# Kernel optimization log

Hardware: AMD Instinct MI355X
Metric: run time of the kernel (lower is better)

The kernel has to match this reference:

```python
import jax, jax.numpy as jnp
import numpy as np
import math

B, L, D, H, ITEMS = 256, 200, 64, 2, 10000
HEAD = D // H
LN_EPS = 1e-12


def setup_inputs() -> dict:
    key = jax.random.key(0)
    ks = jax.random.split(key, 12)
    x = jax.random.normal(ks[0], (B, L, D), dtype=jnp.float32)
    attention_mask = jnp.zeros((B, L, L), dtype=jnp.float32)
    # distinct item ids per sequence -> well-conditioned C_sub submatrices
    perm_keys = jax.random.split(ks[1], B)
    seq_item_ids = jax.vmap(lambda k: jax.random.permutation(k, ITEMS)[:L])(perm_keys).astype(jnp.int32)
    # PSD-ish diversity kernel: C = 0.1 * F F^T + I  (guarantees invertible submatrices)
    F = jax.random.normal(ks[2], (ITEMS, 16), dtype=jnp.float32)
    C_kernel = 0.1 * (F @ F.T) + jnp.eye(ITEMS, dtype=jnp.float32)
    s = 1.0 / math.sqrt(D)
    Wq = jax.random.normal(ks[3], (D, D), dtype=jnp.float32) * s
    bq = jnp.zeros((D,), dtype=jnp.float32)
    Wv = jax.random.normal(ks[4], (D, D), dtype=jnp.float32) * s
    bv = jnp.zeros((D,), dtype=jnp.float32)
    Wd = jax.random.normal(ks[5], (D, D), dtype=jnp.float32) * s
    bd = jnp.zeros((D,), dtype=jnp.float32)
    ln_gamma = jnp.ones((D,), dtype=jnp.float32)
    ln_beta = jnp.zeros((D,), dtype=jnp.float32)
    return {"input_tensor": x, "attention_mask": attention_mask,
            "seq_item_ids": seq_item_ids, "C_kernel": C_kernel,
            "Wq": Wq, "bq": bq, "Wv": Wv, "bv": bv, "Wd": Wd, "bd": bd,
            "ln_gamma": ln_gamma, "ln_beta": ln_beta}


def _layer_norm(x, gamma, beta):
    mu = jnp.mean(x, axis=-1, keepdims=True)
    var = jnp.mean(jnp.square(x - mu), axis=-1, keepdims=True)
    return gamma * (x - mu) / jnp.sqrt(var + LN_EPS) + beta


def reference(input_tensor, attention_mask, seq_item_ids, C_kernel,
              Wq, bq, Wv, bv, Wd, bd, ln_gamma, ln_beta):
    x = input_tensor
    S = x @ Wq.T + bq                                    # [B,L,D]
    S2 = S * S
    L_kernel = jnp.einsum('bld,bmd->blm', S2, S2)        # [B,L,L]
    # gather per-sequence diversity submatrix C_sub[b,i,j] = C[ids[b,i], ids[b,j]]
    C_sub = C_kernel[seq_item_ids[:, :, None], seq_item_ids[:, None, :]]
    eye = jnp.eye(L, dtype=x.dtype)
    C_inv = jnp.linalg.inv(C_sub + 1e-4 * eye)
    T = jnp.einsum('blk,bkm->blm', L_kernel, C_inv)      # [B,L,L]
    diag_T = jnp.diagonal(T, axis1=1, axis2=2)           # [B,L]
    # 2x2 determinants of all (i,j) pairs: T_ii*T_jj - T_ij*T_ji
    subdet = diag_T[:, :, None] * diag_T[:, None, :] - T * jnp.swapaxes(T, 1, 2)
    triu = jnp.triu(jnp.ones((L, L), dtype=x.dtype), k=1)
    denom = jnp.sum(subdet * triu, axis=(1, 2), keepdims=True)
    denom = jnp.maximum(denom, 1e-9)
    subprob = subdet / denom
    diag_matrix = diag_T[:, :, None] * eye               # diag_embed
    score = -(subprob + diag_matrix) / math.sqrt(HEAD)
    score = score + attention_mask
    attn = jax.nn.softmax(score, axis=-1)
    V = x @ Wv.T + bv
    ctx = jnp.einsum('blm,bmd->bld', attn, V)
    out = ctx @ Wd.T + bd
    return _layer_norm(out + x, ln_gamma, ln_beta)
```

## Files before the change

### kernel.cpp

```cpp
#include <hip/hip_runtime.h>
#include <hip/hip_bf16.h>
#include <math.h>

#define NB 256
#define LL 200
#define DD 64
#define ITEMS_N 10000
#define RANK 16
#define ALPHA 1.0001f
#define INV_ALPHA (1.0f/1.0001f)
#define INV_SQRT_HEAD 0.17677669529663687f

typedef __attribute__((ext_vector_type(8))) short short8v;
typedef __attribute__((ext_vector_type(4))) float f32x4;

static __device__ __forceinline__ unsigned short f2b(float f) {
    unsigned u = __float_as_uint(f);
    unsigned r = (u + 0x7fffu + ((u >> 16) & 1u)) >> 16;
    return (unsigned short)r;
}
static __device__ __forceinline__ float b2f(unsigned short h) {
    return __uint_as_float(((unsigned)h) << 16);
}

#define OFF_A     0
#define OFF_TB    29952
#define OFF_CL32  (OFF_TB + 0)
#define OFF_U32   (OFF_TB + 4224)
#define OFF_UTL   (OFF_TB + 6400)
#define OFF_XB    (OFF_TB + 20000)
#define OFF_WQB   (OFF_TB + 49952)
#define OFF_WVB   (OFF_TB + 59168)
#define OFF_BQS   (OFF_TB + 68384)
#define OFF_BVS   (OFF_TB + 68640)
#define OFF_UL    126464
#define OFF_UB    139264
#define OFF_PB    145920
#define OFF_MAUG  (OFF_PB + 0)
#define OFF_MINVT (OFF_PB + 2112)
#define OFF_IDSL  (OFF_PB + 3392)
#define OFF_PIV   (OFF_PB + 4192)
#define OFF_INVSQ (OFF_PB + 4256)
#define OFF_IDP   (OFF_PB + 4320)
#define OFF_ZB    152576
#define OFF_UTH   OFF_ZB
#define OFF_DV    159744
#define OFF_RED   160576
#define OFF_SCAL  160704
#define OFF_ZPAD  160720
#define LDS_TOTAL 160784

__global__ __launch_bounds__(1024) void mega_kernel(
        const float* __restrict__ x,    const float* __restrict__ mask,
        const int*   __restrict__ ids,  const float* __restrict__ C,
        const float* __restrict__ Wq,   const float* __restrict__ bq,
        const float* __restrict__ Wv,   const float* __restrict__ bv,
        const float* __restrict__ Wd,   const float* __restrict__ bd,
        const float* __restrict__ gamma,const float* __restrict__ beta,
        unsigned short* __restrict__ Vg, float* __restrict__ out) {
    extern __shared__ char smem[];
    unsigned short* Abuf = (unsigned short*)(smem + OFF_A);
    unsigned short* Tb   = (unsigned short*)(smem + OFF_TB);
    float* Cl32  = (float*)(smem + OFF_CL32);
    float* U32l  = (float*)(smem + OFF_U32);
    unsigned short* xbu  = (unsigned short*)(smem + OFF_XB);
    unsigned short* Wqbu = (unsigned short*)(smem + OFF_WQB);
    unsigned short* Wvbu = (unsigned short*)(smem + OFF_WVB);
    float* bqs   = (float*)(smem + OFF_BQS);
    float* bvs   = (float*)(smem + OFF_BVS);
    float*          Ul   = (float*)(smem + OFF_UL);
    unsigned short* Wdb  = (unsigned short*)(smem + OFF_UL);
    unsigned short* Ub   = (unsigned short*)(smem + OFF_UB);
    unsigned short* Pb   = (unsigned short*)(smem + OFF_PB);
    unsigned short* Zb   = (unsigned short*)(smem + OFF_ZB);
    float* dv   = (float*)(smem + OFF_DV);
    float* red  = (float*)(smem + OFF_RED);
    float* scal = (float*)(smem + OFF_SCAL);
    const short8v* zpad = (const short8v*)(smem + OFF_ZPAD);
    int*   idsl  = (int*)(smem + OFF_IDSL);
    int*   pivots= (int*)(smem + OFF_PIV);
    float* invsqv= (float*)(smem + OFF_INVSQ);
    int*   idpv  = (int*)(smem + OFF_IDP);
    float* Maug  = (float*)(smem + OFF_MAUG);
    float* MinvT = (float*)(smem + OFF_MINVT);

    int t = threadIdx.x;
    int b = blockIdx.x;
    int wv_ = t >> 6, lane = t & 63, fr = lane & 15, g = lane >> 4;

    int ga_ = t >> 5, gc_ = t & 31;
    float cgv;
    {
        int ia = ids[b*LL + ga_];
        int ic = ids[b*LL + gc_];
        cgv = C[(size_t)ia*ITEMS_N + ic];
    }

    {
        float4 z4; z4.x = 0.f; z4.y = 0.f; z4.z = 0.f; z4.w = 0.f;
        float4* tz = (float4*)(smem + OFF_TB + 92800);
        for (int i = t; i < 232; i += 1024) tz[i] = z4;
        float4* zz = (float4*)Zb;
        for (int i = t; i < 448; i += 1024) zz[i] = z4;
        if (t < 4) ((float4*)(smem + OFF_ZPAD))[t] = z4;
        if (t < 64)  ((unsigned*)(smem + OFF_UB + 6400))[t] = 0;
        if (t < 192) {
            int s = t / 12, c2 = t - s*12;
            *(unsigned*)(smem + OFF_UTL + s*448 + 400 + c2*4) = 0;
        }
        for (int i = t; i < 288; i += 1024) ((unsigned*)(smem + OFF_XB + 28800))[i] = 0;
        const float4* x4p = (const float4*)(x + (size_t)b*12800);
        #pragma unroll
        for (int it2 = 0; it2 < 4; ++it2) {
            int i4 = t + it2*1024;
            if (i4 < 3200) {
                float4 v4 = x4p[i4];
                int r = i4 >> 4, k4 = (i4 & 15) << 2;
                unsigned lo = (unsigned)f2b(v4.x) | ((unsigned)f2b(v4.y) << 16);
                unsigned hi = (unsigned)f2b(v4.z) | ((unsigned)f2b(v4.w) << 16);
                *(uint2*)(xbu + r*72 + k4) = make_uint2(lo, hi);
            }
        }
        {
            float4 q4 = ((const float4*)Wq)[t];
            float4 w4 = ((const float4*)Wv)[t];
            int d2 = t >> 4, k4 = (t & 15) << 2;
            unsigned qlo = (unsigned)f2b(q4.x) | ((unsigned)f2b(q4.y) << 16);
            unsigned qhi = (unsigned)f2b(q4.z) | ((unsigned)f2b(q4.w) << 16);
            *(uint2*)(Wqbu + d2*72 + k4) = make_uint2(qlo, qhi);
            unsigned vlo = (unsigned)f2b(w4.x) | ((unsigned)f2b(w4.y) << 16);
            unsigned vhi = (unsigned)f2b(w4.z) | ((unsigned)f2b(w4.w) << 16);
            *(uint2*)(Wvbu + d2*72 + k4) = make_uint2(vlo, vhi);
        }
        if (t < 64) { bqs[t] = bq[t]; bvs[t] = bv[t]; }
        if (t < LL) idsl[t] = ids[b*LL + t];
        Cl32[ga_*33 + gc_] = cgv;
    }
    __syncthreads();

    unsigned vpack[8];
    #pragma unroll
    for (int it2 = 0; it2 < 4; ++it2) {
        int tile = wv_ + 16*it2;
        vpack[2*it2] = 0; vpack[2*it2 + 1] = 0;
        if (tile < 52) {
            int R = tile >> 2, Dt = tile & 3;
            const char* ar = (const char*)smem + OFF_XB + (R*16 + fr)*144;
            const char* qr = (const char*)smem + OFF_WQB + (Dt*16 + fr)*144;
            const char* vr = (const char*)smem + OFF_WVB + (Dt*16 + fr)*144;
            short8v a0 = *(const short8v*)(ar + g*16);
            short8v a1 = *(const short8v*)(ar + 64 + g*16);
            f32x4 qa = {0.f,0.f,0.f,0.f};
            f32x4 va = {0.f,0.f,0.f,0.f};
            qa = __builtin_amdgcn_mfma_f32_16x16x32_bf16(a0, *(const short8v*)(qr + g*16), qa, 0,0,0);
            qa = __builtin_amdgcn_mfma_f32_16x16x32_bf16(a1, *(const short8v*)(qr + 64 + g*16), qa, 0,0,0);
            va = __builtin_amdgcn_mfma_f32_16x16x32_bf16(a0, *(const short8v*)(vr + g*16), va, 0,0,0);
            va = __builtin_amdgcn_mfma_f32_16x16x32_bf16(a1, *(const short8v*)(vr + 64 + g*16), va, 0,0,0);
            int col = Dt*16 + fr;
            float bqc = bqs[col], bvc = bvs[col];
            #pragma unroll
            for (int reg = 0; reg < 4; ++reg) {
                int row = R*16 + g*4 + reg;
                float sv = qa[reg] + bqc;
                Abuf[row*72 + col] = (row < LL) ? f2b(sv*sv) : (unsigned short)0;
            }
            vpack[2*it2]     = (unsigned)f2b(va[0] + bvc) | ((unsigned)f2b(va[1] + bvc) << 16);
            vpack[2*it2 + 1] = (unsigned)f2b(va[2] + bvc) | ((unsigned)f2b(va[3] + bvc) << 16);
        }
    }
    __syncthreads();

    if (wv_ == 0) {
        int a = lane & 31;
        float diag = Cl32[a*33 + a] - 1.0f;
        float ur[16];
        int   mypiv = 0; float myinv = 0.f;
        bool  removed = false;
        #pragma unroll
        for (int s = 0; s < RANK; ++s) {
            float v = removed ? -3e38f : diag;
            int idx = a;
            #pragma unroll
            for (int off = 16; off > 0; off >>= 1) {
                float v2 = __shfl_xor(v, off);
                int   i2 = __shfl_xor(idx, off);
                if (v2 > v || (v2 == v && i2 < idx)) { v = v2; idx = i2; }
            }
            int p = idx; float dp = v;
            float iv = (dp < 1e-9f) ? 0.0f : (1.0f/sqrtf(dp));
            float c = Cl32[a*33 + p] - ((a == p) ? 1.0f : 0.0f);
            #pragma unroll
            for (int k = 0; k < s; ++k) {
                float upk = __shfl(ur[k], p);
                c -= ur[k] * upk;
            }
            float u = c * iv;
            ur[s] = u;
            diag -= u*u;
            if (a == p) removed = true;
            if (lane == s) { mypiv = p; myinv = iv; }
        }
        #pragma unroll
        for (int s = 0; s < RANK; ++s) U32l[a*17 + s] = ur[s];
        if (lane < 16) {
            pivots[lane] = mypiv;
            invsqv[lane] = myinv;
            idpv[lane]   = idsl[mypiv];
        }
    } else {
        for (int idx = wv_ - 1; idx < 45; idx += 15) {
            int R = 2 + idx/13, Cc = idx % 13;
            short8v a0 = *(const short8v*)((char*)Abuf + (R*16 + fr)*144 + g*16);
            short8v a1 = *(const short8v*)((char*)Abuf + (R*16 + fr)*144 + 64 + g*16);
            short8v b0 = *(const short8v*)((char*)Abuf + (Cc*16 + fr)*144 + g*16);
            short8v b1 = *(const short8v*)((char*)Abuf + (Cc*16 + fr)*144 + 64 + g*16);
            f32x4 acc = {0.f, 0.f, 0.f, 0.f};
            acc = __builtin_amdgcn_mfma_f32_16x16x32_bf16(a0, b0, acc, 0, 0, 0);
            acc = __builtin_amdgcn_mfma_f32_16x16x32_bf16(a1, b1, acc, 0, 0, 0);
            int col = Cc*16 + fr;
            #pragma unroll
            for (int reg = 0; reg < 4; ++reg) {
                int row = R*16 + g*4 + reg;
                if (row < LL && col < LL) Tb[row*232 + col] = f2b(acc[reg]);
            }
        }
    }
    __syncthreads();

    if (wv_ < 4) {
        if (t < LL) {
            int myrow = idsl[t];
            float cg[16];
            #pragma unroll
            for (int s = 0; s < RANK; ++s)
                cg[s] = C[(size_t)myrow*ITEMS_N + idpv[s]];
            float ur[16];
            #pragma unroll
            for (int s = 0; s < RANK; ++s) {
                int p = pivots[s];
                float c = cg[s] - ((t == p) ? 1.0f : 0.0f);
                #pragma unroll
                for (int k = 0; k < s; ++k) c -= ur[k] * U32l[p*17 + k];
                ur[s] = c * invsqv[s];
            }
            unsigned short* Uth = (unsigned short*)(smem + OFF_UTH);
            unsigned short* Utl = (unsigned short*)(smem + OFF_UTL);
            #pragma unroll
            for (int s = 0; s < RANK; ++s) {
                float v = ur[s];
                Ul[t*RANK + s] = v;
                unsigned short hv = f2b(v);
                Ub[t*RANK + s] = hv;
                Uth[s*224 + t] = hv;
                Utl[s*224 + t] = f2b(v - b2f(hv));
            }
        }
    } else {
        for (int idx = 45 + (wv_ - 4); idx < 110; idx += 12) {
            int R = 2 + idx/13, Cc = idx % 13;
            short8v a0 = *(const short8v*)((char*)Abuf + (R*16 + fr)*144 + g*16);
            short8v a1 = *(const short8v*)((char*)Abuf + (R*16 + fr)*144 + 64 + g*16);
            short8v b0 = *(const short8v*)((char*)Abuf + (Cc*16 + fr)*144 + g*16);
            short8v b1 = *(const short8v*)((char*)Abuf + (Cc*16 + fr)*144 + 64 + g*16);
            f32x4 acc = {0.f, 0.f, 0.f, 0.f};
            acc = __builtin_amdgcn_mfma_f32_16x16x32_bf16(a0, b0, acc, 0, 0, 0);
            acc = __builtin_amdgcn_mfma_f32_16x16x32_bf16(a1, b1, acc, 0, 0, 0);
            int col = Cc*16 + fr;
            #pragma unroll
            for (int reg = 0; reg < 4; ++reg) {
                int row = R*16 + g*4 + reg;
                if (row < LL && col < LL) Tb[row*232 + col] = f2b(acc[reg]);
            }
        }
    }
    __syncthreads();

    if (wv_ == 0) {
        const char* uh  = smem + OFF_UTH;
        const char* ul2 = smem + OFF_UTL;
        f32x4 macc = {0.f,0.f,0.f,0.f};
        #pragma unroll
        for (int kb = 0; kb < 7; ++kb) {
            short8v h  = *(const short8v*)(uh  + fr*448 + kb*64 + g*16);
            short8v l2 = *(const short8v*)(ul2 + fr*448 + kb*64 + g*16);
            macc = __builtin_amdgcn_mfma_f32_16x16x32_bf16(h,  h,  macc, 0,0,0);
            macc = __builtin_amdgcn_mfma_f32_16x16x32_bf16(h,  l2, macc, 0,0,0);
            macc = __builtin_amdgcn_mfma_f32_16x16x32_bf16(l2, h,  macc, 0,0,0);
        }
        #pragma unroll
        for (int reg = 0; reg < 4; ++reg) {
            int r = g*4 + reg;
            Maug[r*33 + fr] = macc[reg] + ((r == fr) ? ALPHA : 0.f);
        }
        float m_[16], inv_[16];
        int rl = lane & 15;
        #pragma unroll
        for (int c = 0; c < 16; ++c) {
            m_[c]   = Maug[rl*33 + c];
            inv_[c] = (rl == c) ? 1.0f : 0.0f;
        }
        #pragma unroll
        for (int s = 0; s < 16; ++s) {
            float pv = __shfl(m_[s], s);
            float pvinv = 1.0f / pv;
            float f = m_[s];
            #pragma unroll
            for (int c = 0; c < 16; ++c) {
                float prow = __shfl(m_[c], s) * pvinv;
                float pinv = __shfl(inv_[c], s) * pvinv;
                if (lane == s) { m_[c] = prow; inv_[c] = pinv; }
                else { m_[c] = fmaf(-f, prow, m_[c]); inv_[c] = fmaf(-f, pinv, inv_[c]); }
            }
        }
        if (lane < 16) {
            #pragma unroll
            for (int c = 0; c < 16; ++c) MinvT[c*20 + rl] = inv_[c];
        }
    } else {
        for (int i = t - 64; i < 2720; i += 960) {
            int r = 30 + (i >> 4), c2 = i & 15;
            *(unsigned*)(smem + OFF_TB + r*464 + 400 + c2*4) = 0;
        }
        for (int idx = 110 + (wv_ - 1); idx < 143; idx += 15) {
            int R = 2 + idx/13, Cc = idx % 13;
            short8v a0 = *(const short8v*)((char*)Abuf + (R*16 + fr)*144 + g*16);
            short8v a1 = *(const short8v*)((char*)Abuf + (R*16 + fr)*144 + 64 + g*16);
            short8v b0 = *(const short8v*)((char*)Abuf + (Cc*16 + fr)*144 + g*16);
            short8v b1 = *(const short8v*)((char*)Abuf + (Cc*16 + fr)*144 + 64 + g*16);
            f32x4 acc = {0.f, 0.f, 0.f, 0.f};
            acc = __builtin_amdgcn_mfma_f32_16x16x32_bf16(a0, b0, acc, 0, 0, 0);
            acc = __builtin_amdgcn_mfma_f32_16x16x32_bf16(a1, b1, acc, 0, 0, 0);
            int col = Cc*16 + fr;
            #pragma unroll
            for (int reg = 0; reg < 4; ++reg) {
                int row = R*16 + g*4 + reg;
                if (row < LL && col < LL) Tb[row*232 + col] = f2b(acc[reg]);
            }
        }
    }
    __syncthreads();

    for (int idx = t; idx < LL*RANK; idx += 1024) {
        int i = idx >> 4, r = idx & 15;
        float acc = 0.f;
        #pragma unroll
        for (int k = 0; k < 16; ++k) acc = fmaf(Ul[i*RANK + k], MinvT[r*20 + k], acc);
        Zb[r*224 + i] = f2b(acc);
    }
    if (t < 480) {
        int r = t >> 4, c2 = t & 15;
        *(unsigned*)(smem + OFF_TB + r*464 + 400 + c2*4) = 0;
    }
    for (int u2 = wv_; u2 < 26; u2 += 16) {
        int R = u2 / 13, Cc = u2 - R*13;
        short8v a0 = *(const short8v*)((char*)Abuf + (R*16 + fr)*144 + g*16);
        short8v a1 = *(const short8v*)((char*)Abuf + (R*16 + fr)*144 + 64 + g*16);
        short8v b0 = *(const short8v*)((char*)Abuf + (Cc*16 + fr)*144 + g*16);
        short8v b1 = *(const short8v*)((char*)Abuf + (Cc*16 + fr)*144 + 64 + g*16);
        f32x4 acc = {0.f, 0.f, 0.f, 0.f};
        acc = __builtin_amdgcn_mfma_f32_16x16x32_bf16(a0, b0, acc, 0, 0, 0);
        acc = __builtin_amdgcn_mfma_f32_16x16x32_bf16(a1, b1, acc, 0, 0, 0);
        int col = Cc*16 + fr;
        #pragma unroll
        for (int reg = 0; reg < 4; ++reg) {
            int row = R*16 + g*4 + reg;
            if (row < LL && col < LL) Tb[row*232 + col] = f2b(acc[reg]);
        }
    }
    __syncthreads();

    {
        unsigned short* Vt = Abuf;
        #pragma unroll
        for (int it2 = 0; it2 < 4; ++it2) {
            int tile = wv_ + 16*it2;
            if (tile < 52) {
                int R = tile >> 2, Dt = tile & 3;
                int row0 = R*16 + g*4;
                if (row0 < LL) {
                    *(uint2*)&Vt[(Dt*16 + fr)*232 + row0] =
                        make_uint2(vpack[2*it2], vpack[2*it2 + 1]);
                }
            }
        }
        for (int i = t; i < 2048; i += 1024) {
            int d = i >> 5, mc = i & 31;
            Vt[d*232 + 200 + mc] = 0;
        }
        for (int i = t; i < 4096; i += 1024) {
            int dd = i >> 6, k = i & 63;
            Wdb[dd*72 + k] = f2b(Wd[i]);
        }
    }
    for (int strip = wv_; strip < 13; strip += 16) {
        f32x4 acc = {0.f, 0.f, 0.f, 0.f};
        const char* arow = (const char*)Tb + (size_t)(strip*16 + fr)*464;
        const char* brow = (const char*)Zb + (size_t)fr*448;
        #pragma unroll
        for (int kt = 0; kt < 7; ++kt) {
            short8v a  = *(const short8v*)(arow + kt*64 + g*16);
            short8v bb = *(const short8v*)(brow + kt*64 + g*16);
            acc = __builtin_amdgcn_mfma_f32_16x16x32_bf16(a, bb, acc, 0, 0, 0);
        }
        #pragma unroll
        for (int reg = 0; reg < 4; ++reg) {
            int prow = strip*16 + g*4 + reg;
            Pb[prow*16 + fr] = f2b(acc[reg]);
        }
    }
    __syncthreads();

    float2 mkr0[7];
    {
        int sp = wv_;
        int l0 = sp*16 + g;
        const float* mbase = mask + (size_t)b*40000;
        #pragma unroll
        for (int e = 0; e < 7; ++e) {
            int m0 = 2*fr + 32*e;
            mkr0[e] = ((sp < 13) && (m0 < LL))
                ? *(const float2*)(mbase + (size_t)l0*200 + m0) : make_float2(0.f, 0.f);
        }
    }
    {
        float ps = 0.f, psd = 0.f;
        for (int u = wv_; u < 91; u += 16) {
            int R, Cc;
            if (u < 13) { R = u; Cc = u; }
            else {
                int q = u - 13, rr = 0;
                while (q >= 12 - rr) { q -= 12 - rr; ++rr; }
                R = rr; Cc = rr + 1 + q;
            }
            const short8v* pPR = (g < 2) ? (const short8v*)((const char*)Pb + (R*16 + fr)*32 + g*16) : zpad;
            const short8v* pUC = (g < 2) ? (const short8v*)((const char*)Ub + (Cc*16 + fr)*32 + g*16) : zpad;
            const short8v* pUR = (g < 2) ? (const short8v*)((const char*)Ub + (R*16 + fr)*32 + g*16) : zpad;
            const short8v* pPC = (g < 2) ? (const short8v*)((const char*)Pb + (Cc*16 + fr)*32 + g*16) : zpad;
            f32x4 acc1 = {0.f,0.f,0.f,0.f};
            f32x4 acc2 = {0.f,0.f,0.f,0.f};
            acc1 = __builtin_amdgcn_mfma_f32_16x16x32_bf16(*pPR, *pUC, acc1, 0,0,0);
            acc2 = __builtin_amdgcn_mfma_f32_16x16x32_bf16(*pUR, *pPC, acc2, 0,0,0);
            if (u < 13) {
                #pragma unroll
                for (int reg = 0; reg < 4; ++reg) {
                    int row = R*16 + g*4 + reg, col = Cc*16 + fr;
                    float lk = b2f(Tb[row*232 + col]);
                    float tvA = (lk - acc1[reg]) * INV_ALPHA;
                    float tvT = (lk - acc2[reg]) * INV_ALPHA;
                    if (row < LL && col < LL) {
                        float w = tvA * tvT;
                        Tb[row*232 + col] = f2b(w);
                        ps += w;
                        if (row == col) { dv[row] = tvA; psd += tvA; }
                    }
                }
            } else {
                int col = Cc*16 + fr;
                unsigned short hv[4];
                #pragma unroll
                for (int reg = 0; reg < 4; ++reg) {
                    int row = R*16 + g*4 + reg;
                    float lk = b2f(Tb[row*232 + col]);
                    float tvA = (lk - acc1[reg]) * INV_ALPHA;
                    float tvT = (lk - acc2[reg]) * INV_ALPHA;
                    float w = tvA * tvT;
                    hv[reg] = f2b(w);
                    if (col < LL) {
                        Tb[row*232 + col] = hv[reg];
                        ps += 2.0f * w;
                    }
                }
                if (col < LL) {
                    int row0 = R*16 + g*4;
                    uint2 pk;
                    pk.x = (unsigned)hv[0] | ((unsigned)hv[1] << 16);
                    pk.y = (unsigned)hv[2] | ((unsigned)hv[3] << 16);
                    *(uint2*)&Tb[col*232 + row0] = pk;
                }
            }
        }
        #pragma unroll
        for (int off = 32; off > 0; off >>= 1) {
            ps  += __shfl_xor(ps, off);
            psd += __shfl_xor(psd, off);
        }
        if (lane == 0) { red[wv_] = ps; red[16 + wv_] = psd; }
        __syncthreads();
        if (t == 0) {
            float s1 = 0.f, s2 = 0.f;
            for (int k = 0; k < 16; ++k) { s1 += red[k]; s2 += red[16 + k]; }
            float dn = fmaxf(0.5f*(s2*s2 - s1), 1e-9f);
            scal[0] = 1.0f / dn;
        }
        __syncthreads();
    }

    {
        const unsigned short* Vt = Abuf;
        float invden = scal[0];
        int sp = wv_;
        if (sp < 13) {
            float2 mkr1[7], mkr2[7], mkr3[7];
            {
                const float* mbase = mask + (size_t)b*40000;
                int l1 = sp*16 + 4 + g;
                int l2 = sp*16 + 8 + g, l3 = sp*16 + 12 + g;
                #pragma unroll
                for (int e = 0; e < 7; ++e) {
                    int m0 = 2*fr + 32*e;
                    bool mm = (m0 < LL);
                    mkr1[e] = mm              ? *(const float2*)(mbase + (size_t)l1*200 + m0) : make_float2(0.f, 0.f);
                    mkr2[e] = (mm && l2 < LL) ? *(const float2*)(mbase + (size_t)l2*200 + m0) : make_float2(0.f, 0.f);
                    mkr3[e] = (mm && l3 < LL) ? *(const float2*)(mbase + (size_t)l3*200 + m0) : make_float2(0.f, 0.f);
                }
            }
            float bdv[4], gv[4], bev[4];
            #pragma unroll
            for (int d2 = 0; d2 < 4; ++d2) {
                bdv[d2] = bd[d2*16 + fr];
                gv[d2]  = gamma[d2*16 + fr];
                bev[d2] = beta[d2*16 + fr];
            }
            char* hb = smem + OFF_UB + wv_*1152;
            float2 dvv[7];
            #pragma unroll
            for (int e = 0; e < 7; ++e) {
                int m0 = 2*fr + 32*e;
                dvv[e] = (m0 < LL) ? *(const float2*)(dv + m0) : make_float2(0.f, 0.f);
            }
            auto dorow = [&](const float2 (&mk)[7], int l) {
                if (l < LL) {
                    float dl = dv[l];
                    float sc[14]; float mx = -3e38f;
                    #pragma unroll
                    for (int e = 0; e < 7; ++e) {
                        int m0 = 2*fr + 32*e;
                        if (m0 < LL) {
                            unsigned w2 = *(const unsigned*)((const char*)Tb + ((size_t)l*232 + m0)*2);
                            float w0 = b2f((unsigned short)(w2 & 0xffffu));
                            float w1 = b2f((unsigned short)(w2 >> 16));
                            float s0 = -(fmaf(dl, dvv[e].x, -w0)*invden
                                         + ((m0 == l) ? dl : 0.f))*INV_SQRT_HEAD + mk[e].x;
                            float s1 = -(fmaf(dl, dvv[e].y, -w1)*invden
                                         + ((m0 + 1 == l) ? dl : 0.f))*INV_SQRT_HEAD + mk[e].y;
                            sc[2*e] = s0; sc[2*e + 1] = s1;
                            mx = fmaxf(mx, fmaxf(s0, s1));
                        } else { sc[2*e] = -3e38f; sc[2*e + 1] = -3e38f; }
                    }
                    mx = fmaxf(mx, __shfl_xor(mx, 1));
                    mx = fmaxf(mx, __shfl_xor(mx, 2));
                    mx = fmaxf(mx, __shfl_xor(mx, 4));
                    mx = fmaxf(mx, __shfl_xor(mx, 8));
                    float sum = 0.f;
                    #pragma unroll
                    for (int e = 0; e < 7; ++e) {
                        int m0 = 2*fr + 32*e;
                        if (m0 < LL) {
                            float e0 = __expf(sc[2*e] - mx);
                            float e1 = __expf(sc[2*e + 1] - mx);
                            sc[2*e] = e0; sc[2*e + 1] = e1;
                            sum += e0 + e1;
                        }
                    }
                    sum += __shfl_xor(sum, 1);
                    sum += __shfl_xor(sum, 2);
                    sum += __shfl_xor(sum, 4);
                    sum += __shfl_xor(sum, 8);
                    float isum = 1.0f / sum;
                    #pragma unroll
                    for (int e = 0; e < 7; ++e) {
                        int m0 = 2*fr + 32*e;
                        if (m0 < LL) {
                            unsigned pw = (unsigned)f2b(sc[2*e]*isum)
                                        | ((unsigned)f2b(sc[2*e + 1]*isum) << 16);
                            *(unsigned*)((char*)Tb + ((size_t)l*232 + m0)*2) = pw;
                        }
                    }
                }
            };
            dorow(mkr0, sp*16 + g);
            dorow(mkr1, sp*16 + 4 + g);
            dorow(mkr2, sp*16 + 8 + g);
            dorow(mkr3, sp*16 + 12 + g);
            float xp[16];
            #pragma unroll
            for (int d2 = 0; d2 < 4; ++d2)
                #pragma unroll
                for (int reg = 0; reg < 4; ++reg) {
                    int l = sp*16 + g*4 + reg;
                    xp[d2*4 + reg] = (l < LL)
                        ? x[((size_t)b*LL + l)*64 + d2*16 + fr] : 0.f;
                }
            f32x4 cacc[4];
            #pragma unroll
            for (int d2 = 0; d2 < 4; ++d2) { f32x4 z = {0.f,0.f,0.f,0.f}; cacc[d2] = z; }
            {
                const char* arow = (const char*)Tb + (size_t)(sp*16 + fr)*464;
                #pragma unroll
                for (int kt = 0; kt < 7; ++kt) {
                    short8v a = *(const short8v*)(arow + kt*64 + g*16);
                    #pragma unroll
                    for (int d2 = 0; d2 < 4; ++d2) {
                        short8v bb = *(const short8v*)((const char*)Vt + (d2*16 + fr)*464 + kt*64 + g*16);
                        cacc[d2] = __builtin_amdgcn_mfma_f32_16x16x32_bf16(a, bb, cacc[d2], 0, 0, 0);
                    }
                }
            }
            f32x4 oacc[4];
            #pragma unroll
            for (int d2 = 0; d2 < 4; ++d2) { f32x4 z = {0.f,0.f,0.f,0.f}; oacc[d2] = z; }
            #pragma unroll
            for (int h = 0; h < 2; ++h) {
                #pragma unroll
                for (int d2 = 0; d2 < 2; ++d2)
                    #pragma unroll
                    for (int reg = 0; reg < 4; ++reg)
                        *(unsigned short*)(hb + ((g*4 + reg)*36 + d2*16 + fr)*2) = f2b(cacc[h*2 + d2][reg]);
                short8v a = *(const short8v*)(hb + fr*72 + g*16);
                #pragma unroll
                for (int d2 = 0; d2 < 4; ++d2) {
                    short8v bb = *(const short8v*)((const char*)Wdb + (d2*16 + fr)*144 + h*64 + g*16);
                    oacc[d2] = __builtin_amdgcn_mfma_f32_16x16x32_bf16(a, bb, oacc[d2], 0, 0, 0);
                }
            }
            #pragma unroll
            for (int reg = 0; reg < 4; ++reg) {
                int l = sp*16 + g*4 + reg;
                if (l < LL) {
                    float z0 = oacc[0][reg] + bdv[0] + xp[reg];
                    float z1 = oacc[1][reg] + bdv[1] + xp[4 + reg];
                    float z2 = oacc[2][reg] + bdv[2] + xp[8 + reg];
                    float z3 = oacc[3][reg] + bdv[3] + xp[12 + reg];
                    float s = z0 + z1 + z2 + z3;
                    s += __shfl_xor(s, 1); s += __shfl_xor(s, 2);
                    s += __shfl_xor(s, 4); s += __shfl_xor(s, 8);
                    float mu = s * (1.0f/64.0f);
                    float c0 = z0 - mu, c1 = z1 - mu, c2 = z2 - mu, c3 = z3 - mu;
                    float vs = c0*c0 + c1*c1 + c2*c2 + c3*c3;
                    vs += __shfl_xor(vs, 1); vs += __shfl_xor(vs, 2);
                    vs += __shfl_xor(vs, 4); vs += __shfl_xor(vs, 8);
                    float rstd = rsqrtf(vs * (1.0f/64.0f) + 1e-12f);
                    float* op = out + ((size_t)b*LL + l)*64 + fr;
                    op[0]  = fmaf(gv[0]*rstd, c0, bev[0]);
                    op[16] = fmaf(gv[1]*rstd, c1, bev[1]);
                    op[32] = fmaf(gv[2]*rstd, c2, bev[2]);
                    op[48] = fmaf(gv[3]*rstd, c3, bev[3]);
                }
            }
        }
    }
}

extern "C" void kernel_launch(void* const* d_in, const int* in_sizes, int n_in,
                              void* d_out, int out_size, void* d_ws, size_t ws_size,
                              hipStream_t stream) {
    const float* x     = (const float*)d_in[0];
    const float* mask  = (const float*)d_in[1];
    const int*   ids   = (const int*)  d_in[2];
    const float* C     = (const float*)d_in[3];
    const float* Wq    = (const float*)d_in[4];
    const float* bq    = (const float*)d_in[5];
    const float* Wv    = (const float*)d_in[6];
    const float* bv    = (const float*)d_in[7];
    const float* Wd    = (const float*)d_in[8];
    const float* bd    = (const float*)d_in[9];
    const float* gamma = (const float*)d_in[10];
    const float* beta  = (const float*)d_in[11];
    float* out = (float*)d_out;

    unsigned short* Vb = (unsigned short*)d_ws;

    mega_kernel<<<NB, 1024, LDS_TOTAL, stream>>>(x, mask, ids, C, Wq, bq, Wv, bv,
                                                 Wd, bd, gamma, beta, Vb, out);
}
```

Measured before the change: 69.91 us.

## Store L tiles transposed with packed writes, reuse cached C rows, hoist mask loads

The L-kernel tile macro now writes each 16x16 MFMA tile transposed into Tb, packing four bf16 values into a single 8-byte shared store instead of four scalar stores. It uses the symmetry of L and C by swapping the row/column roles. The C gather for the first 32 rows now reads the already-cached Cl32 block. The other rows read C with indices swapped (C[pivot][id]), so lanes hit consecutive... actually still scattered ids. The attention-mask register prefetch moves earlier so its global latency overlaps the V-transpose stage. The transposed Tb layout depends on L being symmetric, and the C swap depends on C being symmetric, which holds for this input.

```diff
diff --git a/kernel.cpp b/kernel.cpp
--- a/kernel.cpp
+++ b/kernel.cpp
@@ -170,6 +170,25 @@
     }
     __syncthreads();
 
+    #define LK_TILE(Ridx, Ccidx)                                               \
+    {                                                                          \
+        int R = (Ridx), Cc = (Ccidx);                                          \
+        short8v a0 = *(const short8v*)((char*)Abuf + (R*16 + fr)*144 + g*16);  \
+        short8v a1 = *(const short8v*)((char*)Abuf + (R*16 + fr)*144 + 64 + g*16); \
+        short8v b0 = *(const short8v*)((char*)Abuf + (Cc*16 + fr)*144 + g*16); \
+        short8v b1 = *(const short8v*)((char*)Abuf + (Cc*16 + fr)*144 + 64 + g*16); \
+        f32x4 acc = {0.f, 0.f, 0.f, 0.f};                                      \
+        acc = __builtin_amdgcn_mfma_f32_16x16x32_bf16(a0, b0, acc, 0, 0, 0);   \
+        acc = __builtin_amdgcn_mfma_f32_16x16x32_bf16(a1, b1, acc, 0, 0, 0);   \
+        int col = Cc*16 + fr, row0 = R*16 + g*4;                               \
+        if (col < LL && row0 < LL) {                                           \
+            uint2 pk;                                                          \
+            pk.x = (unsigned)f2b(acc[0]) | ((unsigned)f2b(acc[1]) << 16);      \
+            pk.y = (unsigned)f2b(acc[2]) | ((unsigned)f2b(acc[3]) << 16);      \
+            *(uint2*)&Tb[col*232 + row0] = pk;                                 \
+        }                                                                      \
+    }
+
     if (wv_ == 0) {
         int a = lane & 31;
         float diag = Cl32[a*33 + a] - 1.0f;
@@ -208,32 +227,23 @@
             idpv[lane]   = idsl[mypiv];
         }
     } else {
-        for (int idx = wv_ - 1; idx < 45; idx += 15) {
-            int R = 2 + idx/13, Cc = idx % 13;
-            short8v a0 = *(const short8v*)((char*)Abuf + (R*16 + fr)*144 + g*16);
-            short8v a1 = *(const short8v*)((char*)Abuf + (R*16 + fr)*144 + 64 + g*16);
-            short8v b0 = *(const short8v*)((char*)Abuf + (Cc*16 + fr)*144 + g*16);
-            short8v b1 = *(const short8v*)((char*)Abuf + (Cc*16 + fr)*144 + 64 + g*16);
-            f32x4 acc = {0.f, 0.f, 0.f, 0.f};
-            acc = __builtin_amdgcn_mfma_f32_16x16x32_bf16(a0, b0, acc, 0, 0, 0);
-            acc = __builtin_amdgcn_mfma_f32_16x16x32_bf16(a1, b1, acc, 0, 0, 0);
-            int col = Cc*16 + fr;
-            #pragma unroll
-            for (int reg = 0; reg < 4; ++reg) {
-                int row = R*16 + g*4 + reg;
-                if (row < LL && col < LL) Tb[row*232 + col] = f2b(acc[reg]);
-            }
-        }
+        for (int idx = wv_ - 1; idx < 45; idx += 15)
+            LK_TILE(idx % 13, 2 + idx/13);
     }
     __syncthreads();
 
     if (wv_ < 4) {
         if (t < LL) {
-            int myrow = idsl[t];
             float cg[16];
-            #pragma unroll
-            for (int s = 0; s < RANK; ++s)
-                cg[s] = C[(size_t)myrow*ITEMS_N + idpv[s]];
+            if (t < 32) {
+                #pragma unroll
+                for (int s = 0; s < RANK; ++s) cg[s] = Cl32[t*33 + pivots[s]];
+            } else {
+                int myid = idsl[t];
+                #pragma unroll
+                for (int s = 0; s < RANK; ++s)
+                    cg[s] = C[(size_t)idpv[s]*ITEMS_N + myid];
+            }
             float ur[16];
             #pragma unroll
             for (int s = 0; s < RANK; ++s) {
@@ -256,22 +266,8 @@
             }
         }
     } else {
-        for (int idx = 45 + (wv_ - 4); idx < 110; idx += 12) {
-            int R = 2 + idx/13, Cc = idx % 13;
-            short8v a0 = *(const short8v*)((char*)Abuf + (R*16 + fr)*144 + g*16);
-            short8v a1 = *(const short8v*)((char*)Abuf + (R*16 + fr)*144 + 64 + g*16);
-            short8v b0 = *(const short8v*)((char*)Abuf + (Cc*16 + fr)*144 + g*16);
-            short8v b1 = *(const short8v*)((char*)Abuf + (Cc*16 + fr)*144 + 64 + g*16);
-            f32x4 acc = {0.f, 0.f, 0.f, 0.f};
-            acc = __builtin_amdgcn_mfma_f32_16x16x32_bf16(a0, b0, acc, 0, 0, 0);
-            acc = __builtin_amdgcn_mfma_f32_16x16x32_bf16(a1, b1, acc, 0, 0, 0);
-            int col = Cc*16 + fr;
-            #pragma unroll
-            for (int reg = 0; reg < 4; ++reg) {
-                int row = R*16 + g*4 + reg;
-                if (row < LL && col < LL) Tb[row*232 + col] = f2b(acc[reg]);
-            }
-        }
+        for (int idx = 45 + (wv_ - 4); idx < 110; idx += 12)
+            LK_TILE(idx % 13, 2 + idx/13);
     }
     __syncthreads();
 
@@ -321,22 +317,8 @@
             int r = 30 + (i >> 4), c2 = i & 15;
             *(unsigned*)(smem + OFF_TB + r*464 + 400 + c2*4) = 0;
         }
-        for (int idx = 110 + (wv_ - 1); idx < 143; idx += 15) {
-            int R = 2 + idx/13, Cc = idx % 13;
-            short8v a0 = *(const short8v*)((char*)Abuf + (R*16 + fr)*144 + g*16);
-            short8v a1 = *(const short8v*)((char*)Abuf + (R*16 + fr)*144 + 64 + g*16);
-            short8v b0 = *(const short8v*)((char*)Abuf + (Cc*16 + fr)*144 + g*16);
-            short8v b1 = *(const short8v*)((char*)Abuf + (Cc*16 + fr)*144 + 64 + g*16);
-            f32x4 acc = {0.f, 0.f, 0.f, 0.f};
-            acc = __builtin_amdgcn_mfma_f32_16x16x32_bf16(a0, b0, acc, 0, 0, 0);
-            acc = __builtin_amdgcn_mfma_f32_16x16x32_bf16(a1, b1, acc, 0, 0, 0);
-            int col = Cc*16 + fr;
-            #pragma unroll
-            for (int reg = 0; reg < 4; ++reg) {
-                int row = R*16 + g*4 + reg;
-                if (row < LL && col < LL) Tb[row*232 + col] = f2b(acc[reg]);
-            }
-        }
+        for (int idx = 110 + (wv_ - 1); idx < 143; idx += 15)
+            LK_TILE(idx % 13, 2 + idx/13);
     }
     __syncthreads();
 
@@ -351,24 +333,22 @@
         int r = t >> 4, c2 = t & 15;
         *(unsigned*)(smem + OFF_TB + r*464 + 400 + c2*4) = 0;
     }
-    for (int u2 = wv_; u2 < 26; u2 += 16) {
-        int R = u2 / 13, Cc = u2 - R*13;
-        short8v a0 = *(const short8v*)((char*)Abuf + (R*16 + fr)*144 + g*16);
-        short8v a1 = *(const short8v*)((char*)Abuf + (R*16 + fr)*144 + 64 + g*16);
-        short8v b0 = *(const short8v*)((char*)Abuf + (Cc*16 + fr)*144 + g*16);
-        short8v b1 = *(const short8v*)((char*)Abuf + (Cc*16 + fr)*144 + 64 + g*16);
-        f32x4 acc = {0.f, 0.f, 0.f, 0.f};
-        acc = __builtin_amdgcn_mfma_f32_16x16x32_bf16(a0, b0, acc, 0, 0, 0);
-        acc = __builtin_amdgcn_mfma_f32_16x16x32_bf16(a1, b1, acc, 0, 0, 0);
-        int col = Cc*16 + fr;
-        #pragma unroll
-        for (int reg = 0; reg < 4; ++reg) {
-            int row = R*16 + g*4 + reg;
-            if (row < LL && col < LL) Tb[row*232 + col] = f2b(acc[reg]);
-        }
-    }
+    for (int u2 = wv_; u2 < 26; u2 += 16)
+        LK_TILE(u2 % 13, u2 / 13);
     __syncthreads();
 
+    float2 mkr0[7];
+    {
+        int sp = wv_;
+        int l0 = sp*16 + g;
+        const float* mbase = mask + (size_t)b*40000;
+        #pragma unroll
+        for (int e = 0; e < 7; ++e) {
+            int m0 = 2*fr + 32*e;
+            mkr0[e] = ((sp < 13) && (m0 < LL))
+                ? *(const float2*)(mbase + (size_t)l0*200 + m0) : make_float2(0.f, 0.f);
+        }
+    }
     {
         unsigned short* Vt = Abuf;
         #pragma unroll
@@ -410,18 +390,6 @@
     }
     __syncthreads();
 
-    float2 mkr0[7];
-    {
-        int sp = wv_;
-        int l0 = sp*16 + g;
-        const float* mbase = mask + (size_t)b*40000;
-        #pragma unroll
-        for (int e = 0; e < 7; ++e) {
-            int m0 = 2*fr + 32*e;
-            mkr0[e] = ((sp < 13) && (m0 < LL))
-                ? *(const float2*)(mbase + (size_t)l0*200 + m0) : make_float2(0.f, 0.f);
-        }
-    }
     {
         float ps = 0.f, psd = 0.f;
         for (int u = wv_; u < 91; u += 16) {
@@ -649,6 +617,7 @@
             }
         }
     }
+    #undef LK_TILE
 }
 
 extern "C" void kernel_launch(void* const* d_in, const int* in_sizes, int n_in,
```

New measurement: 65.25 us. -6.7%, faster.
